# Kernel tuning notes

Hardware: AMD Instinct MI355X
Metric: run time of the kernel (lower is better)

The kernel has to match this reference:

```python
import jax, jax.numpy as jnp
import numpy as np

LOW_THRESH = 0.3
HIGH_THRESH = 0.7
BATCH_SIZE = 256
NUM_POS = BATCH_SIZE // 2   # 128; guaranteed <= total_pos since B2=512 GT boxes are scattered positive
NUM_NEG = BATCH_SIZE - NUM_POS


def _xcycwh_to_x1y1x2y2(b):
    xc, yc, w, h = b[..., 0], b[..., 1], b[..., 2], b[..., 3]
    return jnp.stack([xc - w / 2, yc - h / 2, xc + w / 2, yc + h / 2], axis=-1)


def box_iou(box1, box2):
    # box1: (1, B1, 4), box2: (1, B2, 4) in (xc, yc, w, h) -> iou (1, B1, B2)
    area1 = box1[..., 2] * box1[..., 3]              # (1, B1)
    area2 = box2[..., 2] * box2[..., 3]              # (1, B2)
    c1 = _xcycwh_to_x1y1x2y2(box1)[:, :, None, :]    # (1, B1, 1, 4)
    c2 = _xcycwh_to_x1y1x2y2(box2)[:, None, :, :]    # (1, 1, B2, 4)
    x0 = jnp.maximum(c1[..., 0], c2[..., 0])
    y0 = jnp.maximum(c1[..., 1], c2[..., 1])
    x1 = jnp.minimum(c1[..., 2], c2[..., 2])
    y1 = jnp.minimum(c1[..., 3], c2[..., 3])
    inter = jnp.maximum(x1 - x0, 0.0) * jnp.maximum(y1 - y0, 0.0)  # (1, B1, B2)
    return inter / (area1[:, :, None] + area2[:, None, :] - inter)


def setup_inputs() -> dict:
    key = jax.random.key(0)
    k1, k2, k3, k4 = jax.random.split(key, 4)
    return {
        "input_boxes": jax.random.uniform(k1, (1, 50000, 4), dtype=jnp.float32),
        "target_boxes": jax.random.uniform(k2, (1, 512, 4), dtype=jnp.float32),
        "pos_noise": jax.random.uniform(k3, (50000,), dtype=jnp.float32),
        "neg_noise": jax.random.uniform(k4, (50000,), dtype=jnp.float32),
    }


def reference(input_boxes, target_boxes, pos_noise, neg_noise):
    ious = box_iou(input_boxes, target_boxes)        # (1, B1, B2)
    input_max_iou = jnp.max(ious, axis=2)            # (1, B1) best GT per proposal
    input_idx = jnp.argmax(ious, axis=2)             # (1, B1)
    target_idx = jnp.argmax(ious, axis=1)            # (1, B2) best proposal per GT

    pos_mask = input_max_iou[0] > HIGH_THRESH        # (B1,)
    neg_mask = input_max_iou[0] < LOW_THRESH
    # each GT's best-matching proposal is forced positive (scatter_)
    pos_mask = pos_mask.at[target_idx[0]].set(True)
    neg_mask = neg_mask.at[target_idx[0]].set(False)
    # fallback: if no negatives at all, negatives = complement of positives
    neg_mask = jnp.where(jnp.sum(neg_mask) == 0, ~pos_mask, neg_mask)

    # uniform sampling without replacement == top-k over iid uniform noise restricted to the mask
    pos_scores = jnp.where(pos_mask, pos_noise, -1.0)
    _, pos_input_idx = jax.lax.top_k(pos_scores, NUM_POS)      # (NUM_POS,)
    neg_scores = jnp.where(neg_mask, neg_noise, -1.0)
    _, neg_input_idx = jax.lax.top_k(neg_scores, NUM_NEG)      # (NUM_NEG,)

    pos_target_idx = input_idx[0][pos_input_idx]               # (NUM_POS,)
    return pos_input_idx, pos_target_idx, neg_input_idx
```

## Files before the change

### kernel.cpp

```cpp
#include <hip/hip_runtime.h>
#include <stdint.h>

#pragma clang fp contract(off)

typedef unsigned long long ull;

#define HIGHT 0.7f
#define LOWT  0.3f
#define KSEL  128
#define CAP   2048
#define MAXGT 512
#define TPB   256
#define CHUNK 32
#define TJ    128
#define SMP   132
#define NLAD  7
#define RB    64

__device__ __constant__ float LADV[NLAD] = {0.998f, 0.99f, 0.95f, 0.8f, 0.5f, 0.25f, 0.0625f};

__device__ __forceinline__ float iou_pair(float ax0, float ay0, float ax1, float ay1, float aarea,
                                          float bx0, float by0, float bx1, float by1, float barea){
#pragma clang fp contract(off)
  float x0 = fmaxf(ax0, bx0);
  float y0 = fmaxf(ay0, by0);
  float x1 = fminf(ax1, bx1);
  float y1 = fminf(ay1, by1);
  float dx = fmaxf(x1 - x0, 0.0f);
  float dy = fmaxf(y1 - y0, 0.0f);
  float inter = dx * dy;
  float uni = (aarea + barea) - inter;
  return inter / uni;
}

__global__ __launch_bounds__(TPB)
void fused_iou(const float4* __restrict__ boxes, const float4* __restrict__ gts,
               int n1, int n2, int nblk,
               float* __restrict__ max_iou, int* __restrict__ input_idx,
               ull* __restrict__ colpart, int* __restrict__ forced,
               int* __restrict__ cnts_part, int* __restrict__ cnts,
               ull* __restrict__ colmax,
               const float* __restrict__ pn, const float* __restrict__ nn)
{
#pragma clang fp contract(off)
  const int b = blockIdx.x, t = threadIdx.x;

  for (int x = b * TPB + t; x < n1; x += nblk * TPB) forced[x] = 0;
  if (b == 0){
    if (t < 32) cnts[t] = 0;
    for (int x = t; x < n2; x += TPB) colmax[x] = 0;
  }

  __shared__ float4 gc[MAXGT];
  __shared__ float  ga[MAXGT];
  __shared__ float  smat[CHUNK * SMP];
  __shared__ float  sm[CHUNK];

  for (int j = t; j < n2; j += TPB){
    float4 g = gts[j];
    float hw = g.z * 0.5f, hh = g.w * 0.5f;
    gc[j] = make_float4(g.x - hw, g.y - hh, g.x + hw, g.y + hh);
    ga[j] = g.z * g.w;
  }
  __syncthreads();

  const int lo = b * CHUNK;
  int cr = n1 - lo; if (cr > CHUNK) cr = CHUNK; if (cr < 0) cr = 0;

  const int pi = t >> 3, q = t & 7;
  const bool valid = (pi < cr);
  float px0 = 0, py0 = 0, px1 = 0, py1 = 0, pa = 0;
  if (valid){
    float4 pb = boxes[lo + pi];
    float hw = pb.z * 0.5f, hh = pb.w * 0.5f;
    px0 = pb.x - hw; py0 = pb.y - hh; px1 = pb.x + hw; py1 = pb.y + hh;
    pa = pb.z * pb.w;
  }
  float vA = -1.0f, vB = -1.0f, vC = -1.0f, vD = -1.0f;
  int jA = 0, jB = 0, jC = 0, jD = 0;

  for (int tb = 0; tb < n2; tb += TJ){
    const int tn = min(TJ, n2 - tb);
    if (valid){
      const int jlim = tb + tn;
      int j0 = tb + q;
      for (; j0 + 24 < jlim; j0 += 32){
        const int ja = j0, jb = j0 + 8, jc = j0 + 16, jd = j0 + 24;
        float4 gA = gc[ja]; float aA = ga[ja];
        float4 gB = gc[jb]; float aB = ga[jb];
        float4 gC = gc[jc]; float aC = ga[jc];
        float4 gD = gc[jd]; float aD = ga[jd];
        float u = iou_pair(px0, py0, px1, py1, pa, gA.x, gA.y, gA.z, gA.w, aA);
        float v = iou_pair(px0, py0, px1, py1, pa, gB.x, gB.y, gB.z, gB.w, aB);
        float w = iou_pair(px0, py0, px1, py1, pa, gC.x, gC.y, gC.z, gC.w, aC);
        float x = iou_pair(px0, py0, px1, py1, pa, gD.x, gD.y, gD.z, gD.w, aD);
        smat[pi * SMP + (ja - tb)] = u;
        smat[pi * SMP + (jb - tb)] = v;
        smat[pi * SMP + (jc - tb)] = w;
        smat[pi * SMP + (jd - tb)] = x;
        if (u > vA){ vA = u; jA = ja; }
        if (v > vB){ vB = v; jB = jb; }
        if (w > vC){ vC = w; jC = jc; }
        if (x > vD){ vD = x; jD = jd; }
      }
      for (; j0 < jlim; j0 += 8){
        float4 g0 = gc[j0]; float a0 = ga[j0];
        float u = iou_pair(px0, py0, px1, py1, pa, g0.x, g0.y, g0.z, g0.w, a0);
        smat[pi * SMP + (j0 - tb)] = u;
        if (u > vA){ vA = u; jA = j0; }
      }
    }
    __syncthreads();
    {
      const int jloc = t >> 1, half = t & 1;
      if (jloc < tn){
        float cv = -1.0f; int cp = 0;
        const int p0 = half * 16;
        const int p1 = min(p0 + 16, cr);
        for (int p = p0; p < p1; ++p){
          float v = smat[p * SMP + jloc];
          if (v > cv){ cv = v; cp = p; }
        }
        float ov = __shfl_xor(cv, 1, 64);
        int   op = __shfl_xor(cp, 1, 64);
        if (ov > cv || (ov == cv && op < cp)){ cv = ov; cp = op; }
        if (half == 0){
          colpart[(size_t)b * n2 + (tb + jloc)] =
            ((ull)__float_as_uint(cv) << 32) | (ull)(unsigned)~(unsigned)(lo + cp);
        }
      }
    }
    __syncthreads();
  }

  if (vB > vA || (vB == vA && jB < jA)){ vA = vB; jA = jB; }
  if (vC > vA || (vC == vA && jC < jA)){ vA = vC; jA = jC; }
  if (vD > vA || (vD == vA && jD < jA)){ vA = vD; jA = jD; }
  #pragma unroll
  for (int m = 1; m <= 4; m <<= 1){
    float ov = __shfl_xor(vA, m, 64);
    int   oj = __shfl_xor(jA, m, 64);
    if (ov > vA || (ov == vA && oj < jA)){ vA = ov; jA = oj; }
  }
  if (valid && q == 0){
    max_iou[lo + pi] = vA;
    input_idx[lo + pi] = jA;
    sm[pi] = vA;
  }
  __syncthreads();

  if (t < 64){
    const bool vld = (t < cr);
    float m = vld ? sm[t] : -1.0f;
    bool pos = vld && (m > HIGHT);
    bool nm  = vld && (m < LOWT);
    bool np  = vld && !(m > HIGHT);
    float sp = pos ? pn[lo + t] : -1.0f;
    float sn = (nm || np) ? nn[lo + t] : -1.0f;
    int c[24];
    c[0] = __popcll(__ballot(pos));
    c[1] = __popcll(__ballot(nm));
    c[2] = __popcll(__ballot(np));
    #pragma unroll
    for (int k = 0; k < NLAD; ++k){
      float L = LADV[k];
      c[3 + k]  = __popcll(__ballot(pos && sp > L));
      c[10 + k] = __popcll(__ballot(nm  && sn > L));
      c[17 + k] = __popcll(__ballot(np  && sn > L));
    }
    if (t == 0){
      #pragma unroll
      for (int k = 0; k < 24; ++k) cnts_part[b * 24 + k] = c[k];
    }
  }
}

__global__ __launch_bounds__(256)
void colreduce(const ull* __restrict__ colpart, int n1, int n2, int nblk,
               const float* __restrict__ max_iou,
               const float* __restrict__ pn, const float* __restrict__ nn,
               int* __restrict__ forced, const int* __restrict__ cnts_part,
               int* __restrict__ cnts, ull* __restrict__ colmax)
{
  const int t = threadIdx.x, b = blockIdx.x, nb = gridDim.x;

  for (int j = t; j < n2; j += 256){
    ull m = 0;
    for (int x = b; x < nblk; x += nb){
      ull v = colpart[(size_t)x * n2 + j];
      if (v > m) m = v;
    }
    if (m) atomicMax(&colmax[j], m);
  }
  if (t < 24){
    int s = 0;
    for (int x = b; x < nblk; x += nb) s += cnts_part[x * 24 + t];
    if (s) atomicAdd(&cnts[t], s);
  }

  __threadfence();
  __shared__ int islast;
  if (t == 0) islast = (atomicAdd(&cnts[26], 1) == nb - 1) ? 1 : 0;
  __syncthreads();
  if (!islast) return;
  __threadfence();

  for (int j = t; j < n2; j += 256){
    ull key = __hip_atomic_load(&colmax[j], __ATOMIC_RELAXED, __HIP_MEMORY_SCOPE_AGENT);
    unsigned idx = ~(unsigned)(key & 0xFFFFFFFFull);
    if (idx < (unsigned)n1){
      int old = atomicExch(&forced[idx], 1);
      if (old == 0){
        float m2 = max_iou[idx];
        if (!(m2 > HIGHT)){
          float sp = pn[idx];
          float sn = nn[idx];
          atomicAdd(&cnts[0], 1);
          atomicAdd(&cnts[2], -1);
          #pragma unroll
          for (int k = 0; k < NLAD; ++k){
            float L = LADV[k];
            if (sp > L) atomicAdd(&cnts[3 + k], 1);
            if (sn > L) atomicAdd(&cnts[17 + k], -1);
          }
          if (m2 < LOWT){
            atomicAdd(&cnts[1], -1);
            #pragma unroll
            for (int k = 0; k < NLAD; ++k)
              if (sn > LADV[k]) atomicAdd(&cnts[10 + k], -1);
          }
        }
      }
    }
  }
}

__device__ __forceinline__ float pick_tau(const int* lad, int tot){
  if (tot <= CAP) return -1.0f;
  for (int k = 0; k < NLAD; ++k)
    if (lad[k] >= KSEL) return LADV[k];
  return -1.0f;
}

__global__ __launch_bounds__(TPB)
void collect_kernel(const float* __restrict__ max_iou, const int* __restrict__ forced,
                    const float* __restrict__ pn, const float* __restrict__ nn,
                    int n1, int* __restrict__ cnts, ull* __restrict__ cand)
{
  __shared__ int s_c[24];
  const int t = threadIdx.x;
  if (t < 24) s_c[t] = cnts[t];
  __syncthreads();
  const bool fb = (s_c[1] == 0);
  const int totP = s_c[0];
  const int totN = fb ? s_c[2] : s_c[1];
  const float tauP = pick_tau(&s_c[3], totP);
  const float tauN = pick_tau(fb ? &s_c[17] : &s_c[10], totN);

  const int i = blockIdx.x * TPB + t;
  if (i >= n1) return;
  float m = max_iou[i];
  bool f = forced[i] != 0;
  bool pos = (m > HIGHT) || f;
  if (pos){
    float sc = pn[i];
    if (sc > tauP){
      int p = atomicAdd(&cnts[24], 1);
      if (p < CAP) cand[p] = ((ull)(__float_as_uint(sc) + 1u) << 32) | (ull)(unsigned)~(unsigned)i;
    }
  } else if (totP < KSEL && i < 2 * KSEL){
    int p = atomicAdd(&cnts[24], 1);
    if (p < CAP) cand[p] = (ull)(unsigned)~(unsigned)i;
  }
  bool seln = fb ? (!pos) : ((m < LOWT) && !f);
  if (seln){
    float sc = nn[i];
    if (sc > tauN){
      int p = atomicAdd(&cnts[25], 1);
      if (p < CAP) cand[CAP + p] = ((ull)(__float_as_uint(sc) + 1u) << 32) | (ull)(unsigned)~(unsigned)i;
    }
  } else if (totN < KSEL && i < 2 * KSEL){
    int p = atomicAdd(&cnts[25], 1);
    if (p < CAP) cand[CAP + p] = (ull)(unsigned)~(unsigned)i;
  }
}

__global__ __launch_bounds__(1024)
void select_kernel(const ull* __restrict__ cand, const int* __restrict__ cnts,
                   const int* __restrict__ input_idx, int* __restrict__ out)
{
  const int t = threadIdx.x;
  const bool isPos = (blockIdx.x == 0);
  __shared__ ull keys[CAP];
  int n = cnts[isPos ? 24 : 25]; if (n > CAP) n = CAP;
  for (int x = t; x < n; x += 1024)
    keys[x] = cand[(isPos ? 0 : CAP) + x];
  __syncthreads();
  ull mk[2]; int mr[2]; int ne = 0;
  for (int x = t; x < n; x += 1024){ mk[ne] = keys[x]; mr[ne] = 0; ++ne; }
  for (int o = 0; o < n; ++o){
    ull ko = keys[o];
    if (ne > 0) mr[0] += (ko > mk[0]);
    if (ne > 1) mr[1] += (ko > mk[1]);
  }
  for (int e = 0; e < ne; ++e){
    int r = mr[e];
    if (r < KSEL){
      unsigned idx = ~(unsigned)(mk[e] & 0xFFFFFFFFull);
      if (isPos){ out[r] = (int)idx; out[KSEL + r] = input_idx[idx]; }
      else        out[2 * KSEL + r] = (int)idx;
    }
  }
}

extern "C" void kernel_launch(void* const* d_in, const int* in_sizes, int n_in,
                              void* d_out, int out_size, void* d_ws, size_t ws_size,
                              hipStream_t stream){
  const float4* boxes = (const float4*)d_in[0];
  const float4* gts   = (const float4*)d_in[1];
  const float* pos_noise = (const float*)d_in[2];
  const float* neg_noise = (const float*)d_in[3];
  const int n1 = in_sizes[0] / 4;
  const int n2 = in_sizes[1] / 4;
  int* out = (int*)d_out;

  char* ws = (char*)d_ws;
  size_t off = 0;
  auto carve = [&](size_t bytes) -> char* {
    char* p = ws + off;
    off = (off + bytes + 255) & ~(size_t)255;
    return p;
  };
  const int nblk = (n1 + CHUNK - 1) / CHUNK;
  float* max_iou   = (float*)carve((size_t)n1 * 4);
  int*   input_idx = (int*)  carve((size_t)n1 * 4);
  ull*   colpart   = (ull*)  carve((size_t)nblk * n2 * 8);
  int*   forced    = (int*)  carve((size_t)n1 * 4);
  int*   cnts_part = (int*)  carve((size_t)nblk * 24 * 4);
  int*   cnts      = (int*)  carve(32 * 4);
  ull*   colmax    = (ull*)  carve((size_t)MAXGT * 8);
  ull*   cand      = (ull*)  carve((size_t)2 * CAP * 8);

  const int gb = (n1 + TPB - 1) / TPB;
  fused_iou<<<nblk, TPB, 0, stream>>>(boxes, gts, n1, n2, nblk,
                                      max_iou, input_idx, colpart, forced,
                                      cnts_part, cnts, colmax, pos_noise, neg_noise);
  colreduce<<<RB, 256, 0, stream>>>(colpart, n1, n2, nblk, max_iou,
                                    pos_noise, neg_noise, forced, cnts_part, cnts, colmax);
  collect_kernel<<<gb, TPB, 0, stream>>>(max_iou, forced, pos_noise, neg_noise,
                                         n1, cnts, cand);
  select_kernel<<<2, 1024, 0, stream>>>(cand, cnts, input_idx, out);
}
```

Before: 151.5 us.

## Fuse column reduce, collect and select kernels into one with grid-wide spin barriers

Merges the three post-IoU kernels (colreduce, collect, select) into a single finish_kernel launched with 98 blocks of 512 threads. Blocks are ordered through global atomic counters and spin-waits instead of kernel boundaries, and the work is redistributed: every block takes part in the column reduction, and the select step runs with 512 threads each ranking 4 keys. The aim is to remove two kernel launch gaps and their drain and fill time. In exchange, the spin barriers depend on all blocks being resident at once, and the column reduction is now split across many more blocks, which means more atomics per column.

```diff
diff --git a/kernel.cpp b/kernel.cpp
--- a/kernel.cpp
+++ b/kernel.cpp
@@ -11,11 +11,11 @@
 #define CAP   2048
 #define MAXGT 512
 #define TPB   256
+#define TPBF  512
 #define CHUNK 32
 #define TJ    128
 #define SMP   132
 #define NLAD  7
-#define RB    64
 
 __device__ __constant__ float LADV[NLAD] = {0.998f, 0.99f, 0.95f, 0.8f, 0.5f, 0.25f, 0.0625f};
 
@@ -175,66 +175,6 @@
   }
 }
 
-__global__ __launch_bounds__(256)
-void colreduce(const ull* __restrict__ colpart, int n1, int n2, int nblk,
-               const float* __restrict__ max_iou,
-               const float* __restrict__ pn, const float* __restrict__ nn,
-               int* __restrict__ forced, const int* __restrict__ cnts_part,
-               int* __restrict__ cnts, ull* __restrict__ colmax)
-{
-  const int t = threadIdx.x, b = blockIdx.x, nb = gridDim.x;
-
-  for (int j = t; j < n2; j += 256){
-    ull m = 0;
-    for (int x = b; x < nblk; x += nb){
-      ull v = colpart[(size_t)x * n2 + j];
-      if (v > m) m = v;
-    }
-    if (m) atomicMax(&colmax[j], m);
-  }
-  if (t < 24){
-    int s = 0;
-    for (int x = b; x < nblk; x += nb) s += cnts_part[x * 24 + t];
-    if (s) atomicAdd(&cnts[t], s);
-  }
-
-  __threadfence();
-  __shared__ int islast;
-  if (t == 0) islast = (atomicAdd(&cnts[26], 1) == nb - 1) ? 1 : 0;
-  __syncthreads();
-  if (!islast) return;
-  __threadfence();
-
-  for (int j = t; j < n2; j += 256){
-    ull key = __hip_atomic_load(&colmax[j], __ATOMIC_RELAXED, __HIP_MEMORY_SCOPE_AGENT);
-    unsigned idx = ~(unsigned)(key & 0xFFFFFFFFull);
-    if (idx < (unsigned)n1){
-      int old = atomicExch(&forced[idx], 1);
-      if (old == 0){
-        float m2 = max_iou[idx];
-        if (!(m2 > HIGHT)){
-          float sp = pn[idx];
-          float sn = nn[idx];
-          atomicAdd(&cnts[0], 1);
-          atomicAdd(&cnts[2], -1);
-          #pragma unroll
-          for (int k = 0; k < NLAD; ++k){
-            float L = LADV[k];
-            if (sp > L) atomicAdd(&cnts[3 + k], 1);
-            if (sn > L) atomicAdd(&cnts[17 + k], -1);
-          }
-          if (m2 < LOWT){
-            atomicAdd(&cnts[1], -1);
-            #pragma unroll
-            for (int k = 0; k < NLAD; ++k)
-              if (sn > LADV[k]) atomicAdd(&cnts[10 + k], -1);
-          }
-        }
-      }
-    }
-  }
-}
-
 __device__ __forceinline__ float pick_tau(const int* lad, int tot){
   if (tot <= CAP) return -1.0f;
   for (int k = 0; k < NLAD; ++k)
@@ -242,14 +182,77 @@
   return -1.0f;
 }
 
-__global__ __launch_bounds__(TPB)
-void collect_kernel(const float* __restrict__ max_iou, const int* __restrict__ forced,
-                    const float* __restrict__ pn, const float* __restrict__ nn,
-                    int n1, int* __restrict__ cnts, ull* __restrict__ cand)
+__global__ __launch_bounds__(TPBF)
+void finish_kernel(const ull* __restrict__ colpart, int n1, int n2, int nblk,
+                   const float* __restrict__ max_iou, const int* __restrict__ input_idx,
+                   const float* __restrict__ pn, const float* __restrict__ nn,
+                   int* __restrict__ forced, const int* __restrict__ cnts_part,
+                   int* __restrict__ cnts, ull* __restrict__ colmax,
+                   ull* __restrict__ cand, int* __restrict__ out)
 {
+  const int t = threadIdx.x, b = blockIdx.x, nb = gridDim.x;
+
+  for (int j = t; j < n2; j += TPBF){
+    ull m = 0;
+    for (int x = b; x < nblk; x += nb){
+      ull v = colpart[(size_t)x * n2 + j];
+      if (v > m) m = v;
+    }
+    if (m) atomicMax(&colmax[j], m);
+  }
+  if (t < 24){
+    int s = 0;
+    for (int x = b; x < nblk; x += nb) s += cnts_part[x * 24 + t];
+    if (s) atomicAdd(&cnts[t], s);
+  }
+
+  __shared__ int islast;
+  __threadfence();
+  __syncthreads();
+  if (t == 0) islast = (atomicAdd(&cnts[26], 1) == nb - 1) ? 1 : 0;
+  __syncthreads();
+  if (islast){
+    for (int j = t; j < n2; j += TPBF){
+      ull key = __hip_atomic_load(&colmax[j], __ATOMIC_RELAXED, __HIP_MEMORY_SCOPE_AGENT);
+      unsigned idx = ~(unsigned)(key & 0xFFFFFFFFull);
+      if (idx < (unsigned)n1){
+        int old = atomicExch(&forced[idx], 1);
+        if (old == 0){
+          float m2 = max_iou[idx];
+          if (!(m2 > HIGHT)){
+            float sp = pn[idx];
+            float sn = nn[idx];
+            atomicAdd(&cnts[0], 1);
+            atomicAdd(&cnts[2], -1);
+            #pragma unroll
+            for (int k = 0; k < NLAD; ++k){
+              float L = LADV[k];
+              if (sp > L) atomicAdd(&cnts[3 + k], 1);
+              if (sn > L) atomicAdd(&cnts[17 + k], -1);
+            }
+            if (m2 < LOWT){
+              atomicAdd(&cnts[1], -1);
+              #pragma unroll
+              for (int k = 0; k < NLAD; ++k)
+                if (sn > LADV[k]) atomicAdd(&cnts[10 + k], -1);
+            }
+          }
+        }
+      }
+    }
+    __threadfence();
+    __syncthreads();
+    if (t == 0) __hip_atomic_store(&cnts[27], 1, __ATOMIC_RELEASE, __HIP_MEMORY_SCOPE_AGENT);
+  }
+  if (t == 0){
+    while (__hip_atomic_load(&cnts[27], __ATOMIC_RELAXED, __HIP_MEMORY_SCOPE_AGENT) == 0)
+      __builtin_amdgcn_s_sleep(1);
+  }
+  __syncthreads();
+  __threadfence();
+
   __shared__ int s_c[24];
-  const int t = threadIdx.x;
-  if (t < 24) s_c[t] = cnts[t];
+  if (t < 24) s_c[t] = __hip_atomic_load(&cnts[t], __ATOMIC_RELAXED, __HIP_MEMORY_SCOPE_AGENT);
   __syncthreads();
   const bool fb = (s_c[1] == 0);
   const int totP = s_c[0];
@@ -257,58 +260,79 @@
   const float tauP = pick_tau(&s_c[3], totP);
   const float tauN = pick_tau(fb ? &s_c[17] : &s_c[10], totN);
 
-  const int i = blockIdx.x * TPB + t;
-  if (i >= n1) return;
-  float m = max_iou[i];
-  bool f = forced[i] != 0;
-  bool pos = (m > HIGHT) || f;
-  if (pos){
-    float sc = pn[i];
-    if (sc > tauP){
+  const int i = b * TPBF + t;
+  if (i < n1){
+    float m = max_iou[i];
+    bool f = __hip_atomic_load(&forced[i], __ATOMIC_RELAXED, __HIP_MEMORY_SCOPE_AGENT) != 0;
+    bool pos = (m > HIGHT) || f;
+    if (pos){
+      float sc = pn[i];
+      if (sc > tauP){
+        int p = atomicAdd(&cnts[24], 1);
+        if (p < CAP)
+          __hip_atomic_store(&cand[p], ((ull)(__float_as_uint(sc) + 1u) << 32) | (ull)(unsigned)~(unsigned)i,
+                             __ATOMIC_RELAXED, __HIP_MEMORY_SCOPE_AGENT);
+      }
+    } else if (totP < KSEL && i < 2 * KSEL){
       int p = atomicAdd(&cnts[24], 1);
-      if (p < CAP) cand[p] = ((ull)(__float_as_uint(sc) + 1u) << 32) | (ull)(unsigned)~(unsigned)i;
-    }
-  } else if (totP < KSEL && i < 2 * KSEL){
-    int p = atomicAdd(&cnts[24], 1);
-    if (p < CAP) cand[p] = (ull)(unsigned)~(unsigned)i;
-  }
-  bool seln = fb ? (!pos) : ((m < LOWT) && !f);
-  if (seln){
-    float sc = nn[i];
-    if (sc > tauN){
+      if (p < CAP)
+        __hip_atomic_store(&cand[p], (ull)(unsigned)~(unsigned)i,
+                           __ATOMIC_RELAXED, __HIP_MEMORY_SCOPE_AGENT);
+    }
+    bool seln = fb ? (!pos) : ((m < LOWT) && !f);
+    if (seln){
+      float sc = nn[i];
+      if (sc > tauN){
+        int p = atomicAdd(&cnts[25], 1);
+        if (p < CAP)
+          __hip_atomic_store(&cand[CAP + p], ((ull)(__float_as_uint(sc) + 1u) << 32) | (ull)(unsigned)~(unsigned)i,
+                             __ATOMIC_RELAXED, __HIP_MEMORY_SCOPE_AGENT);
+      }
+    } else if (totN < KSEL && i < 2 * KSEL){
       int p = atomicAdd(&cnts[25], 1);
-      if (p < CAP) cand[CAP + p] = ((ull)(__float_as_uint(sc) + 1u) << 32) | (ull)(unsigned)~(unsigned)i;
-    }
-  } else if (totN < KSEL && i < 2 * KSEL){
-    int p = atomicAdd(&cnts[25], 1);
-    if (p < CAP) cand[CAP + p] = (ull)(unsigned)~(unsigned)i;
-  }
-}
-
-__global__ __launch_bounds__(1024)
-void select_kernel(const ull* __restrict__ cand, const int* __restrict__ cnts,
-                   const int* __restrict__ input_idx, int* __restrict__ out)
-{
-  const int t = threadIdx.x;
-  const bool isPos = (blockIdx.x == 0);
+      if (p < CAP)
+        __hip_atomic_store(&cand[CAP + p], (ull)(unsigned)~(unsigned)i,
+                           __ATOMIC_RELAXED, __HIP_MEMORY_SCOPE_AGENT);
+    }
+  }
+
+  __threadfence();
+  __syncthreads();
+  if (t == 0) atomicAdd(&cnts[28], 1);
+  if (b >= 2) return;
+  if (t == 0){
+    while (__hip_atomic_load(&cnts[28], __ATOMIC_RELAXED, __HIP_MEMORY_SCOPE_AGENT) != nb)
+      __builtin_amdgcn_s_sleep(1);
+  }
+  __syncthreads();
+  __threadfence();
+
+  const bool isPos = (b == 0);
   __shared__ ull keys[CAP];
-  int n = cnts[isPos ? 24 : 25]; if (n > CAP) n = CAP;
-  for (int x = t; x < n; x += 1024)
-    keys[x] = cand[(isPos ? 0 : CAP) + x];
-  __syncthreads();
-  ull mk[2]; int mr[2]; int ne = 0;
-  for (int x = t; x < n; x += 1024){ mk[ne] = keys[x]; mr[ne] = 0; ++ne; }
+  int n = __hip_atomic_load(&cnts[isPos ? 24 : 25], __ATOMIC_RELAXED, __HIP_MEMORY_SCOPE_AGENT);
+  if (n > CAP) n = CAP;
+  for (int x = t; x < n; x += TPBF)
+    keys[x] = __hip_atomic_load(&cand[(isPos ? 0 : CAP) + x], __ATOMIC_RELAXED, __HIP_MEMORY_SCOPE_AGENT);
+  __syncthreads();
+  ull mk[4]; int mr[4];
+  #pragma unroll
+  for (int e = 0; e < 4; ++e){
+    int x = t + e * TPBF;
+    mk[e] = (x < n) ? keys[x] : ~0ull;
+    mr[e] = 0;
+  }
   for (int o = 0; o < n; ++o){
     ull ko = keys[o];
-    if (ne > 0) mr[0] += (ko > mk[0]);
-    if (ne > 1) mr[1] += (ko > mk[1]);
-  }
-  for (int e = 0; e < ne; ++e){
-    int r = mr[e];
-    if (r < KSEL){
+    #pragma unroll
+    for (int e = 0; e < 4; ++e) mr[e] += (ko > mk[e]);
+  }
+  #pragma unroll
+  for (int e = 0; e < 4; ++e){
+    int x = t + e * TPBF;
+    if (x < n && mr[e] < KSEL){
       unsigned idx = ~(unsigned)(mk[e] & 0xFFFFFFFFull);
-      if (isPos){ out[r] = (int)idx; out[KSEL + r] = input_idx[idx]; }
-      else        out[2 * KSEL + r] = (int)idx;
+      if (isPos){ out[mr[e]] = (int)idx; out[KSEL + mr[e]] = input_idx[idx]; }
+      else        out[2 * KSEL + mr[e]] = (int)idx;
     }
   }
 }
@@ -341,13 +365,11 @@
   ull*   colmax    = (ull*)  carve((size_t)MAXGT * 8);
   ull*   cand      = (ull*)  carve((size_t)2 * CAP * 8);
 
-  const int gb = (n1 + TPB - 1) / TPB;
   fused_iou<<<nblk, TPB, 0, stream>>>(boxes, gts, n1, n2, nblk,
                                       max_iou, input_idx, colpart, forced,
                                       cnts_part, cnts, colmax, pos_noise, neg_noise);
-  colreduce<<<RB, 256, 0, stream>>>(colpart, n1, n2, nblk, max_iou,
-                                    pos_noise, neg_noise, forced, cnts_part, cnts, colmax);
-  collect_kernel<<<gb, TPB, 0, stream>>>(max_iou, forced, pos_noise, neg_noise,
-                                         n1, cnts, cand);
-  select_kernel<<<2, 1024, 0, stream>>>(cand, cnts, input_idx, out);
-}
+  const int fbk = (n1 + TPBF - 1) / TPBF;
+  finish_kernel<<<fbk, TPBF, 0, stream>>>(colpart, n1, n2, nblk, max_iou, input_idx,
+                                          pos_noise, neg_noise, forced, cnts_part,
+                                          cnts, colmax, cand, out);
+}
```

After: 167.5 us. 10.6% more time.

## Split column reduction into separate kernel and drop last-block fence handoff

Applied to the files above, without the earlier changes.

Replaces the column-max reduction kernel, which used a last-block-done atomic handoff with thread fences, by two kernels. The first is a 96-block reduction in which each thread handles two fixed columns. The second is a single-block kernel that applies the forced-positive fixes. The select kernel is also restructured to use fixed unrolled per-thread slots with sentinel keys. This trades the fence and serialized tail work for one extra kernel launch. It also assumes n2 is at most 512.

```diff
diff --git a/kernel.cpp b/kernel.cpp
--- a/kernel.cpp
+++ b/kernel.cpp
@@ -15,7 +15,7 @@
 #define TJ    128
 #define SMP   132
 #define NLAD  7
-#define RB    64
+#define NRB   96
 
 __device__ __constant__ float LADV[NLAD] = {0.998f, 0.99f, 0.95f, 0.8f, 0.5f, 0.25f, 0.0625f};
 
@@ -175,63 +175,61 @@
   }
 }
 
-__global__ __launch_bounds__(256)
-void colreduce(const ull* __restrict__ colpart, int n1, int n2, int nblk,
-               const float* __restrict__ max_iou,
-               const float* __restrict__ pn, const float* __restrict__ nn,
-               int* __restrict__ forced, const int* __restrict__ cnts_part,
-               int* __restrict__ cnts, ull* __restrict__ colmax)
-{
-  const int t = threadIdx.x, b = blockIdx.x, nb = gridDim.x;
-
-  for (int j = t; j < n2; j += 256){
-    ull m = 0;
-    for (int x = b; x < nblk; x += nb){
-      ull v = colpart[(size_t)x * n2 + j];
-      if (v > m) m = v;
-    }
-    if (m) atomicMax(&colmax[j], m);
-  }
+__global__ __launch_bounds__(TPB)
+void colreduce2(const ull* __restrict__ colpart, int n2, int nblk,
+                const int* __restrict__ cnts_part,
+                int* __restrict__ cnts, ull* __restrict__ colmax)
+{
+  const int t = threadIdx.x, b = blockIdx.x;
+  ull m0 = 0, m1 = 0;
+  const int c0 = t, c1 = t + TPB;
+  for (int x = b; x < nblk; x += NRB){
+    const ull* row = colpart + (size_t)x * n2;
+    ull v0 = row[c0];
+    ull v1 = (c1 < n2) ? row[c1] : 0;
+    if (v0 > m0) m0 = v0;
+    if (v1 > m1) m1 = v1;
+  }
+  if (c0 < n2 && m0) atomicMax(&colmax[c0], m0);
+  if (c1 < n2 && m1) atomicMax(&colmax[c1], m1);
+
   if (t < 24){
     int s = 0;
-    for (int x = b; x < nblk; x += nb) s += cnts_part[x * 24 + t];
+    for (int x = b; x < nblk; x += NRB) s += cnts_part[x * 24 + t];
     if (s) atomicAdd(&cnts[t], s);
   }
-
-  __threadfence();
-  __shared__ int islast;
-  if (t == 0) islast = (atomicAdd(&cnts[26], 1) == nb - 1) ? 1 : 0;
-  __syncthreads();
-  if (!islast) return;
-  __threadfence();
-
-  for (int j = t; j < n2; j += 256){
-    ull key = __hip_atomic_load(&colmax[j], __ATOMIC_RELAXED, __HIP_MEMORY_SCOPE_AGENT);
-    unsigned idx = ~(unsigned)(key & 0xFFFFFFFFull);
-    if (idx < (unsigned)n1){
-      int old = atomicExch(&forced[idx], 1);
-      if (old == 0){
-        float m2 = max_iou[idx];
-        if (!(m2 > HIGHT)){
-          float sp = pn[idx];
-          float sn = nn[idx];
-          atomicAdd(&cnts[0], 1);
-          atomicAdd(&cnts[2], -1);
-          #pragma unroll
-          for (int k = 0; k < NLAD; ++k){
-            float L = LADV[k];
-            if (sp > L) atomicAdd(&cnts[3 + k], 1);
-            if (sn > L) atomicAdd(&cnts[17 + k], -1);
-          }
-          if (m2 < LOWT){
-            atomicAdd(&cnts[1], -1);
-            #pragma unroll
-            for (int k = 0; k < NLAD; ++k)
-              if (sn > LADV[k]) atomicAdd(&cnts[10 + k], -1);
-          }
-        }
-      }
-    }
+}
+
+__global__ __launch_bounds__(512)
+void forcefix(const ull* __restrict__ colmax, int n1, int n2,
+              const float* __restrict__ max_iou,
+              const float* __restrict__ pn, const float* __restrict__ nn,
+              int* __restrict__ forced, int* __restrict__ cnts)
+{
+  const int t = threadIdx.x;
+  if (t >= n2) return;
+  ull key = colmax[t];
+  unsigned idx = ~(unsigned)(key & 0xFFFFFFFFull);
+  if (idx >= (unsigned)n1) return;
+  int old = atomicExch(&forced[idx], 1);
+  if (old != 0) return;
+  float m2 = max_iou[idx];
+  if (m2 > HIGHT) return;
+  float sp = pn[idx];
+  float sn = nn[idx];
+  atomicAdd(&cnts[0], 1);
+  atomicAdd(&cnts[2], -1);
+  #pragma unroll
+  for (int k = 0; k < NLAD; ++k){
+    float L = LADV[k];
+    if (sp > L) atomicAdd(&cnts[3 + k], 1);
+    if (sn > L) atomicAdd(&cnts[17 + k], -1);
+  }
+  if (m2 < LOWT){
+    atomicAdd(&cnts[1], -1);
+    #pragma unroll
+    for (int k = 0; k < NLAD; ++k)
+      if (sn > LADV[k]) atomicAdd(&cnts[10 + k], -1);
   }
 }
 
@@ -296,19 +294,25 @@
   for (int x = t; x < n; x += 1024)
     keys[x] = cand[(isPos ? 0 : CAP) + x];
   __syncthreads();
-  ull mk[2]; int mr[2]; int ne = 0;
-  for (int x = t; x < n; x += 1024){ mk[ne] = keys[x]; mr[ne] = 0; ++ne; }
+  ull mk[2]; int mr[2];
+  #pragma unroll
+  for (int e = 0; e < 2; ++e){
+    int x = t + e * 1024;
+    mk[e] = (x < n) ? keys[x] : ~0ull;
+    mr[e] = 0;
+  }
   for (int o = 0; o < n; ++o){
     ull ko = keys[o];
-    if (ne > 0) mr[0] += (ko > mk[0]);
-    if (ne > 1) mr[1] += (ko > mk[1]);
-  }
-  for (int e = 0; e < ne; ++e){
-    int r = mr[e];
-    if (r < KSEL){
+    #pragma unroll
+    for (int e = 0; e < 2; ++e) mr[e] += (ko > mk[e]);
+  }
+  #pragma unroll
+  for (int e = 0; e < 2; ++e){
+    int x = t + e * 1024;
+    if (x < n && mr[e] < KSEL){
       unsigned idx = ~(unsigned)(mk[e] & 0xFFFFFFFFull);
-      if (isPos){ out[r] = (int)idx; out[KSEL + r] = input_idx[idx]; }
-      else        out[2 * KSEL + r] = (int)idx;
+      if (isPos){ out[mr[e]] = (int)idx; out[KSEL + mr[e]] = input_idx[idx]; }
+      else        out[2 * KSEL + mr[e]] = (int)idx;
     }
   }
 }
@@ -345,8 +349,9 @@
   fused_iou<<<nblk, TPB, 0, stream>>>(boxes, gts, n1, n2, nblk,
                                       max_iou, input_idx, colpart, forced,
                                       cnts_part, cnts, colmax, pos_noise, neg_noise);
-  colreduce<<<RB, 256, 0, stream>>>(colpart, n1, n2, nblk, max_iou,
-                                    pos_noise, neg_noise, forced, cnts_part, cnts, colmax);
+  colreduce2<<<NRB, TPB, 0, stream>>>(colpart, n2, nblk, cnts_part, cnts, colmax);
+  forcefix<<<1, 512, 0, stream>>>(colmax, n1, n2, max_iou,
+                                  pos_noise, neg_noise, forced, cnts);
   collect_kernel<<<gb, TPB, 0, stream>>>(max_iou, forced, pos_noise, neg_noise,
                                          n1, cnts, cand);
   select_kernel<<<2, 1024, 0, stream>>>(cand, cnts, input_idx, out);
```

Measured after the change: 130.7 us. 1.16x faster.
